# Kernel optimization log

Measured on AMD Instinct MI355X. Metric: run time of the kernel, lower is better.

## Reference

```python
import jax, jax.numpy as jnp
import numpy as np

B = 4; S_L = 512; WIN = 256; SCH = 3; CCH = 128; F = 8; P = 4; RNN = 128; FC = 256
L1 = (WIN - F + 1) // P          # after conv1 + pool1
L2 = (L1 - F + 1) // P           # after conv2 + pool2
D1 = L2 * CCH                    # flattened conv feature dim fed to GRU


def _conv1d(x, w, b):
    # x: (N, W, Cin), w: (F, Cin, Cout), VALID, stride 1 (matches keras Conv1D)
    return jax.lax.conv_general_dilated(x, w, (1,), 'VALID', dimension_numbers=('NWC', 'WIO', 'NWC')) + b


def _maxpool(x, p):
    return jax.lax.reduce_window(x, -jnp.inf, jax.lax.max, (1, p, 1), (1, p, 1), 'VALID')


def _gru(x, h0, mask, W, U, b):
    # keras GRU v2 (reset_after=True). b[0]=input bias, b[1]=recurrent bias.
    # Masked steps carry state through (keras semantics: output==state for GRU).
    u = U.shape[0]
    xg = x @ W + b[0]  # (B, T, 3u) precomputed input projections
    br = b[1]

    def step(h, inp):
        xt, mt = inp  # (B, 3u), (B,)
        rg = h @ U + br
        z = jax.nn.sigmoid(xt[:, :u] + rg[:, :u])
        r = jax.nn.sigmoid(xt[:, u:2 * u] + rg[:, u:2 * u])
        hh = jnp.tanh(xt[:, 2 * u:] + r * rg[:, 2 * u:])
        hn = z * h + (1.0 - z) * hh
        hn = jnp.where(mt[:, None], hn, h)
        return hn, hn

    _, ys = jax.lax.scan(step, h0, (jnp.swapaxes(xg, 0, 1), jnp.swapaxes(mask, 0, 1)))
    return jnp.swapaxes(ys, 0, 1)  # (B, T, u)


def _bidir(x, m, hf, hb, Wf, Uf, bf, Wb, Ub, bb):
    # Bidirectional(merge='concat'); backward layer sees reversed inputs+mask,
    # its output is reversed back to align with time (keras behaviour).
    yf = _gru(x, hf, m, Wf, Uf, bf)
    yb = _gru(x[:, ::-1], hb, m[:, ::-1], Wb, Ub, bb)[:, ::-1]
    return jnp.concatenate([yf, yb], axis=-1)


def _forward(x, state1_f, state1_b, state2_f, state2_b,
             conv1_w, conv1_b, conv2_w, conv2_b,
             g1f_W, g1f_U, g1f_b, g1b_W, g1b_U, g1b_b,
             g2f_W, g2f_U, g2f_b, g2b_W, g2b_U, g2b_b,
             d1_w, d1_b, d2_w, d2_b, d3_w, d3_b, m):
    bsz = x.shape[0]
    h = x.reshape(bsz * S_L, WIN, SCH)
    h = _maxpool(jax.nn.leaky_relu(_conv1d(h, conv1_w, conv1_b), 0.2), P)
    h = _maxpool(jax.nn.leaky_relu(_conv1d(h, conv2_w, conv2_b), 0.2), P)
    h = h.reshape(bsz, S_L, D1)
    h = _bidir(h, m, state1_f, state1_b, g1f_W, g1f_U, g1f_b, g1b_W, g1b_U, g1b_b)
    h = _bidir(h, m, state2_f, state2_b, g2f_W, g2f_U, g2f_b, g2b_W, g2b_U, g2b_b)
    # keras layers.Attention(use_scale=False): dot-product self attention,
    # key mask -> -1e9 on scores, query mask -> zero outputs.
    scores = jnp.einsum('btd,bsd->bts', h, h)
    scores = jnp.where(m[:, None, :], scores, -1e9)
    h = jnp.einsum('bts,bsd->btd', jax.nn.softmax(scores, axis=-1), h)
    h = h * m[:, :, None].astype(h.dtype)
    h = jax.nn.leaky_relu(h @ d1_w + d1_b, 0.2)   # dropout is identity at inference
    h = jax.nn.leaky_relu(h @ d2_w + d2_b, 0.2)
    return (h @ d3_w + d3_b)[..., 0]              # squeeze -> (B, s_l)


def setup_inputs() -> dict:
    key = jax.random.key(0)
    ks = jax.random.split(key, 32)
    g = lambda k, s: jax.random.normal(k, s, jnp.float32) * 0.05
    inp = {}
    inp['x'] = jax.random.normal(ks[0], (B, S_L, WIN, SCH), jnp.float32)
    inp['m'] = jax.random.randint(ks[1], (B, S_L), 0, 2) > 0
    inp['state1_f'] = jax.random.uniform(ks[2], (B, RNN), jnp.float32, -1.0, 1.0)
    inp['state1_b'] = jax.random.uniform(ks[3], (B, RNN), jnp.float32, -1.0, 1.0)
    inp['state2_f'] = jax.random.uniform(ks[4], (B, RNN), jnp.float32, -1.0, 1.0)
    inp['state2_b'] = jax.random.uniform(ks[5], (B, RNN), jnp.float32, -1.0, 1.0)
    inp['conv1_w'] = g(ks[6], (F, SCH, CCH)); inp['conv1_b'] = jnp.zeros((CCH,), jnp.float32)
    inp['conv2_w'] = g(ks[7], (F, CCH, CCH)); inp['conv2_b'] = jnp.zeros((CCH,), jnp.float32)
    i = 8
    for nm, din in (('g1f', D1), ('g1b', D1), ('g2f', 2 * RNN), ('g2b', 2 * RNN)):
        inp[nm + '_W'] = g(ks[i], (din, 3 * RNN))
        inp[nm + '_U'] = g(ks[i + 1], (RNN, 3 * RNN))
        inp[nm + '_b'] = jnp.zeros((2, 3 * RNN), jnp.float32)
        i += 2
    inp['d1_w'] = g(ks[i], (2 * RNN, FC)); inp['d1_b'] = jnp.zeros((FC,), jnp.float32)
    inp['d2_w'] = g(ks[i + 1], (FC, FC)); inp['d2_b'] = jnp.zeros((FC,), jnp.float32)
    inp['d3_w'] = g(ks[i + 2], (FC, 1)); inp['d3_b'] = jnp.zeros((1,), jnp.float32)
    return inp


def reference(x, m, state1_f, state1_b, state2_f, state2_b,
              conv1_w, conv1_b, conv2_w, conv2_b,
              g1f_W, g1f_U, g1f_b, g1b_W, g1b_U, g1b_b,
              g2f_W, g2f_U, g2f_b, g2b_W, g2b_U, g2b_b,
              d1_w, d1_b, d2_w, d2_b, d3_w, d3_b):
    return _forward(x, state1_f, state1_b, state2_f, state2_b,
                    conv1_w, conv1_b, conv2_w, conv2_b,
                    g1f_W, g1f_U, g1f_b, g1b_W, g1b_U, g1b_b,
                    g2f_W, g2f_U, g2f_b, g2b_W, g2b_U, g2b_b,
                    d1_w, d1_b, d2_w, d2_b, d3_w, d3_b, m)
```

## Files before the change

### kernel.cpp

```cpp
#include <hip/hip_runtime.h>

#define LRELU(v) ((v) > 0.f ? (v) : 0.2f * (v))

typedef float f32x4 __attribute__((ext_vector_type(4)));
typedef __bf16 bf16x8 __attribute__((ext_vector_type(8)));
typedef unsigned short ushort8v __attribute__((ext_vector_type(8)));
typedef unsigned int u32x2 __attribute__((ext_vector_type(2)));

__device__ __forceinline__ unsigned short f2bf(float f) {
    unsigned int u = __float_as_uint(f);
    u += 0x7fffu + ((u >> 16) & 1u);
    return (unsigned short)(u >> 16);
}
__device__ __forceinline__ float bf2f(unsigned short h) {
    return __uint_as_float(((unsigned int)h) << 16);
}
__device__ __forceinline__ float sigmoid_fast(float x) {
    float e = __builtin_amdgcn_exp2f(-x * 1.442695041f);
    return __builtin_amdgcn_rcpf(1.f + e);
}
__device__ __forceinline__ float tanh_fast(float x) {
    float e = __builtin_amdgcn_exp2f(x * 2.885390082f);
    return 1.f - 2.f * __builtin_amdgcn_rcpf(e + 1.f);
}
__device__ __forceinline__ float dpp_add_xor1(float v) {
    int r = __builtin_amdgcn_mov_dpp(__float_as_int(v), 0xB1, 0xF, 0xF, true);
    return v + __int_as_float(r);
}
__device__ __forceinline__ float dpp_add_xor2(float v) {
    int r = __builtin_amdgcn_mov_dpp(__float_as_int(v), 0x4E, 0xF, 0xF, true);
    return v + __int_as_float(r);
}

__device__ __forceinline__ void wtpack(const float* __restrict__ W,
                                       unsigned short* __restrict__ h,
                                       unsigned short* __restrict__ l, int K,
                                       int N, long idx) {
    int n = (int)(idx / K), k = (int)(idx % K);
    float v = W[(long)k * N + n];
    unsigned short hi = f2bf(v);
    h[idx] = hi;
    l[idx] = f2bf(v - bf2f(hi));
}
__device__ __forceinline__ void ugpack(const float* __restrict__ U,
                                       float* __restrict__ up, int widx) {
    int t = widx / 96;
    int rem = widx % 96;
    int j = rem >> 2, i = rem & 3;
    int g = j >> 3, q = j & 7;
    int c = t >> 2, kq = t & 3;
    up[widx] = U[(long)(kq * 32 + q * 4 + i) * 384 + g * 128 + c];
}

__global__ __launch_bounds__(256) void prepack_all(
    const float* __restrict__ w2, unsigned short* __restrict__ bth,
    unsigned short* __restrict__ btl, const float* __restrict__ g1fW,
    unsigned short* __restrict__ wt1fh, unsigned short* __restrict__ wt1fl,
    const float* __restrict__ g1bW, unsigned short* __restrict__ wt1bh,
    unsigned short* __restrict__ wt1bl, const float* __restrict__ g2fW,
    unsigned short* __restrict__ wt2fh, unsigned short* __restrict__ wt2fl,
    const float* __restrict__ g2bW, unsigned short* __restrict__ wt2bh,
    unsigned short* __restrict__ wt2bl, const float* __restrict__ g1fU,
    float* __restrict__ up1f, const float* __restrict__ g1bU,
    float* __restrict__ up1b, const float* __restrict__ g2fU,
    float* __restrict__ up2f, const float* __restrict__ g2bU,
    float* __restrict__ up2b, const unsigned int* __restrict__ mraw,
    int* __restrict__ mi) {
    const int bid = blockIdx.x, tid = threadIdx.x;
    if (bid < 512) {
        int idx = bid * 256 + tid;
        int c = idx >> 10, k = idx & 1023;
        float v = w2[k * 128 + c];
        unsigned short hi = f2bf(v);
        bth[(long)c * 1024 + k] = hi;
        btl[(long)c * 1024 + k] = f2bf(v - bf2f(hi));
    } else if (bid < 3008) {
        wtpack(g1fW, wt1fh, wt1fl, 1664, 384, (long)(bid - 512) * 256 + tid);
    } else if (bid < 5504) {
        wtpack(g1bW, wt1bh, wt1bl, 1664, 384, (long)(bid - 3008) * 256 + tid);
    } else if (bid < 5888) {
        wtpack(g2fW, wt2fh, wt2fl, 256, 384, (long)(bid - 5504) * 256 + tid);
    } else if (bid < 6272) {
        wtpack(g2bW, wt2bh, wt2bl, 256, 384, (long)(bid - 5888) * 256 + tid);
    } else if (bid < 6464) {
        ugpack(g1fU, up1f, (bid - 6272) * 256 + tid);
    } else if (bid < 6656) {
        ugpack(g1bU, up1b, (bid - 6464) * 256 + tid);
    } else if (bid < 6848) {
        ugpack(g2fU, up2f, (bid - 6656) * 256 + tid);
    } else if (bid < 7040) {
        ugpack(g2bU, up2b, (bid - 6848) * 256 + tid);
    } else {
        __shared__ int flag;
        if (tid == 0) flag = 0;
        __syncthreads();
        unsigned a = mraw[tid * 2], bb = mraw[tid * 2 + 1];
        if (a > 1u || bb > 1u) flag = 1;
        __syncthreads();
        if (flag) {
            const unsigned char* b8 = (const unsigned char*)mraw;
            for (int i = tid; i < 2048; i += 256) mi[i] = b8[i] ? 1 : 0;
        } else {
            for (int i = tid; i < 2048; i += 256) mi[i] = mraw[i] ? 1 : 0;
        }
    }
}

__global__ __launch_bounds__(256) void conv_kernel(
    const float* __restrict__ x, const float* __restrict__ w1,
    const float* __restrict__ b1, const unsigned short* __restrict__ bth,
    const unsigned short* __restrict__ btl, const float* __restrict__ b2,
    unsigned short* __restrict__ feat_h, unsigned short* __restrict__ feat_l) {
    __shared__ float xs[3][256];
    __shared__ __align__(16) unsigned short p1h[72 * 128];
    __shared__ __align__(16) unsigned short p1l[72 * 128];
    long s = blockIdx.x;
    int tid = threadIdx.x;
    const float* xp = x + s * 768;
    for (int i = tid; i < 768; i += 256) xs[i % 3][i / 3] = xp[i];
    for (int i = tid; i < 10 * 128; i += 256) {
        p1h[62 * 128 + i] = 0;
        p1l[62 * 128 + i] = 0;
    }
    __syncthreads();

    {
        int ch = tid & 127;
        int half = tid >> 7;
        float w1r[24];
#pragma unroll
        for (int fc = 0; fc < 24; fc++) w1r[fc] = w1[fc * 128 + ch];
        float bias1 = b1[ch];
        for (int po = half; po < 62; po += 2) {
            int p0 = po * 4;
            float a0 = bias1, a1 = bias1, a2 = bias1, a3 = bias1;
#pragma unroll
            for (int c = 0; c < 3; c++) {
                float xv[11];
#pragma unroll
                for (int q = 0; q < 11; q++) xv[q] = xs[c][p0 + q];
#pragma unroll
                for (int f = 0; f < 8; f++) {
                    float w = w1r[f * 3 + c];
                    a0 = fmaf(xv[f + 0], w, a0);
                    a1 = fmaf(xv[f + 1], w, a1);
                    a2 = fmaf(xv[f + 2], w, a2);
                    a3 = fmaf(xv[f + 3], w, a3);
                }
            }
            float m01 = fmaxf(LRELU(a0), LRELU(a1));
            float m23 = fmaxf(LRELU(a2), LRELU(a3));
            float v = fmaxf(m01, m23);
            unsigned short hi = f2bf(v);
            unsigned short lo = f2bf(v - bf2f(hi));
            int cs = ch ^ ((po & 7) << 3);
            p1h[po * 128 + cs] = hi;
            p1l[po * 128 + cs] = lo;
        }
    }
    __syncthreads();

    const int l = tid & 63, w = tid >> 6;
    const int r = l & 15, g = l >> 4;
    f32x4 acc[4][2];
    const f32x4 zz = {0.f, 0.f, 0.f, 0.f};
#pragma unroll
    for (int m = 0; m < 4; m++) {
        acc[m][0] = zz;
        acc[m][1] = zz;
    }
#pragma unroll 2
    for (int ks = 0; ks < 32; ks++) {
        const int f = ks >> 2;
        const int cin0 = ((ks & 3) << 5) + (g << 3);
        bf16x8 bh[2], bl[2];
#pragma unroll
        for (int n = 0; n < 2; n++) {
            const int c = ((w << 1) + n) * 16 + r;
            const long bo = (long)c * 1024 + (ks << 5) + (g << 3);
            bh[n] = __builtin_bit_cast(bf16x8, *(const ushort8v*)(bth + bo));
            bl[n] = __builtin_bit_cast(bf16x8, *(const ushort8v*)(btl + bo));
        }
        bf16x8 ah[4], al[4];
#pragma unroll
        for (int m = 0; m < 4; m++) {
            const int row = m * 16 + r + f;
            const int col = cin0 ^ ((row & 7) << 3);
            const int off = row * 128 + col;
            ah[m] = __builtin_bit_cast(bf16x8, *(const ushort8v*)(p1h + off));
            al[m] = __builtin_bit_cast(bf16x8, *(const ushort8v*)(p1l + off));
        }
#pragma unroll
        for (int m = 0; m < 4; m++) {
#pragma unroll
            for (int n = 0; n < 2; n++) {
                acc[m][n] = __builtin_amdgcn_mfma_f32_16x16x32_bf16(ah[m], bh[n], acc[m][n], 0, 0, 0);
                acc[m][n] = __builtin_amdgcn_mfma_f32_16x16x32_bf16(ah[m], bl[n], acc[m][n], 0, 0, 0);
                acc[m][n] = __builtin_amdgcn_mfma_f32_16x16x32_bf16(al[m], bh[n], acc[m][n], 0, 0, 0);
            }
        }
    }
#pragma unroll
    for (int m = 0; m < 4; m++) {
        const int j = m * 4 + g;
        if (j < 13) {
#pragma unroll
            for (int n = 0; n < 2; n++) {
                const int ch = ((w << 1) + n) * 16 + r;
                const float bias = b2[ch];
                float v0 = LRELU(acc[m][n].x + bias);
                float v1 = LRELU(acc[m][n].y + bias);
                float v2 = LRELU(acc[m][n].z + bias);
                float v3 = LRELU(acc[m][n].w + bias);
                float v = fmaxf(fmaxf(v0, v1), fmaxf(v2, v3));
                unsigned short hi = f2bf(v);
                feat_h[s * 1664 + j * 128 + ch] = hi;
                feat_l[s * 1664 + j * 128 + ch] = f2bf(v - bf2f(hi));
            }
        }
    }
}

__global__ __launch_bounds__(256) void gemm_proj(
    const unsigned short* __restrict__ Agh, const unsigned short* __restrict__ Agl,
    const unsigned short* __restrict__ B0h, const unsigned short* __restrict__ B0l,
    const unsigned short* __restrict__ B1h, const unsigned short* __restrict__ B1l,
    const float* __restrict__ bias0, const float* __restrict__ bias1,
    float* __restrict__ C0, float* __restrict__ C1, int M, int N, int K) {
    const int z = blockIdx.z;
    const unsigned short* __restrict__ Bth = z ? B1h : B0h;
    const unsigned short* __restrict__ Btl = z ? B1l : B0l;
    const float* __restrict__ bias = z ? bias1 : bias0;
    float* __restrict__ C = z ? C1 : C0;
    __shared__ __align__(16) unsigned short Ahs[2][64 * 32];
    __shared__ __align__(16) unsigned short Als[2][64 * 32];
    const int tid = threadIdx.x;
    const int w = tid >> 6, l = tid & 63, r = l & 15, g = l >> 4;
    const int m0 = blockIdx.y * 64, n0 = blockIdx.x * 64;
    const int col = n0 + w * 16 + r;
    const int srow = tid >> 2, sgq = tid & 3;
    f32x4 acc[4];
    const f32x4 zzv = {0.f, 0.f, 0.f, 0.f};
#pragma unroll
    for (int m = 0; m < 4; m++) acc[m] = zzv;

    const long abase = (long)(m0 + srow) * K + ((sgq ^ (srow & 3)) << 3);
    auto stage = [&](int k0, int buf) {
        __builtin_amdgcn_global_load_lds(
            (const __attribute__((address_space(1))) void*)(Agh + abase + k0),
            (__attribute__((address_space(3))) void*)&Ahs[buf][tid * 8], 16, 0, 0);
        __builtin_amdgcn_global_load_lds(
            (const __attribute__((address_space(1))) void*)(Agl + abase + k0),
            (__attribute__((address_space(3))) void*)&Als[buf][tid * 8], 16, 0, 0);
    };
    stage(0, 0);
    const long bbase = (long)col * K + g * 8;
    ushort8v bhc = *(const ushort8v*)(Bth + bbase);
    ushort8v blc = *(const ushort8v*)(Btl + bbase);

    for (int k0 = 0; k0 < K; k0 += 32) {
        const int buf = (k0 >> 5) & 1;
        asm volatile("s_waitcnt vmcnt(0)" ::: "memory");
        __builtin_amdgcn_s_barrier();
        ushort8v nbh, nbl;
        if (k0 + 32 < K) {
            stage(k0 + 32, buf ^ 1);
            nbh = *(const ushort8v*)(Bth + bbase + k0 + 32);
            nbl = *(const ushort8v*)(Btl + bbase + k0 + 32);
        }
        bf16x8 bh = __builtin_bit_cast(bf16x8, bhc);
        bf16x8 bl = __builtin_bit_cast(bf16x8, blc);
#pragma unroll
        for (int m = 0; m < 4; m++) {
            const int arow = m * 16 + r;
            const int aoff = arow * 32 + ((g ^ (arow & 3)) << 3);
            bf16x8 ah = __builtin_bit_cast(bf16x8, *(const ushort8v*)(&Ahs[buf][aoff]));
            bf16x8 al = __builtin_bit_cast(bf16x8, *(const ushort8v*)(&Als[buf][aoff]));
            acc[m] = __builtin_amdgcn_mfma_f32_16x16x32_bf16(ah, bh, acc[m], 0, 0, 0);
            acc[m] = __builtin_amdgcn_mfma_f32_16x16x32_bf16(ah, bl, acc[m], 0, 0, 0);
            acc[m] = __builtin_amdgcn_mfma_f32_16x16x32_bf16(al, bh, acc[m], 0, 0, 0);
        }
        bhc = nbh;
        blc = nbl;
    }
    const float bv = bias[col];
#pragma unroll
    for (int m = 0; m < 4; m++) {
#pragma unroll
        for (int q = 0; q < 4; q++) {
            const int row = m0 + m * 16 + g * 4 + q;
            C[(long)row * N + col] = acc[m][q] + bv;
        }
    }
}

__global__ __launch_bounds__(256) void gemm_scores(
    const unsigned short* __restrict__ Hh, const unsigned short* __restrict__ Hl,
    const int* __restrict__ mask, float* __restrict__ S) {
    const int bz = blockIdx.z;
    const unsigned short* __restrict__ Agh = Hh + (long)bz * 512 * 256;
    const unsigned short* __restrict__ Agl = Hl + (long)bz * 512 * 256;
    float* __restrict__ C = S + (long)bz * 512 * 512;
    const int K = 256, N = 512;
    __shared__ __align__(16) unsigned short Ahs[2][64 * 32];
    __shared__ __align__(16) unsigned short Als[2][64 * 32];
    const int tid = threadIdx.x;
    const int w = tid >> 6, l = tid & 63, r = l & 15, g = l >> 4;
    const int m0 = blockIdx.y * 64, n0 = blockIdx.x * 64;
    const int col = n0 + w * 16 + r;
    const int srow = tid >> 2, sgq = tid & 3;
    f32x4 acc[4];
    const f32x4 zzv = {0.f, 0.f, 0.f, 0.f};
#pragma unroll
    for (int m = 0; m < 4; m++) acc[m] = zzv;

    const long abase = (long)(m0 + srow) * K + ((sgq ^ (srow & 3)) << 3);
    auto stage = [&](int k0, int buf) {
        __builtin_amdgcn_global_load_lds(
            (const __attribute__((address_space(1))) void*)(Agh + abase + k0),
            (__attribute__((address_space(3))) void*)&Ahs[buf][tid * 8], 16, 0, 0);
        __builtin_amdgcn_global_load_lds(
            (const __attribute__((address_space(1))) void*)(Agl + abase + k0),
            (__attribute__((address_space(3))) void*)&Als[buf][tid * 8], 16, 0, 0);
    };
    stage(0, 0);
    const long bbase = (long)col * K + g * 8;
    ushort8v bhc = *(const ushort8v*)(Agh + bbase);
    ushort8v blc = *(const ushort8v*)(Agl + bbase);

    for (int k0 = 0; k0 < K; k0 += 32) {
        const int buf = (k0 >> 5) & 1;
        asm volatile("s_waitcnt vmcnt(0)" ::: "memory");
        __builtin_amdgcn_s_barrier();
        ushort8v nbh, nbl;
        if (k0 + 32 < K) {
            stage(k0 + 32, buf ^ 1);
            nbh = *(const ushort8v*)(Agh + bbase + k0 + 32);
            nbl = *(const ushort8v*)(Agl + bbase + k0 + 32);
        }
        bf16x8 bh = __builtin_bit_cast(bf16x8, bhc);
        bf16x8 bl = __builtin_bit_cast(bf16x8, blc);
#pragma unroll
        for (int m = 0; m < 4; m++) {
            const int arow = m * 16 + r;
            const int aoff = arow * 32 + ((g ^ (arow & 3)) << 3);
            bf16x8 ah = __builtin_bit_cast(bf16x8, *(const ushort8v*)(&Ahs[buf][aoff]));
            bf16x8 al = __builtin_bit_cast(bf16x8, *(const ushort8v*)(&Als[buf][aoff]));
            acc[m] = __builtin_amdgcn_mfma_f32_16x16x32_bf16(ah, bh, acc[m], 0, 0, 0);
            acc[m] = __builtin_amdgcn_mfma_f32_16x16x32_bf16(ah, bl, acc[m], 0, 0, 0);
            acc[m] = __builtin_amdgcn_mfma_f32_16x16x32_bf16(al, bh, acc[m], 0, 0, 0);
        }
        bhc = nbh;
        blc = nbl;
    }
    const int mk = mask[bz * 512 + col];
#pragma unroll
    for (int m = 0; m < 4; m++) {
#pragma unroll
        for (int q = 0; q < 4; q++) {
            const int row = m0 + m * 16 + g * 4 + q;
            float v = acc[m][q];
            C[(long)row * N + col] = mk ? v : -1e9f;
        }
    }
}

template <int ACT>
__global__ __launch_bounds__(256) void gemm_nn(
    const float* __restrict__ A, long sA, const float* __restrict__ B, long sB,
    const float* __restrict__ bias, const int* __restrict__ qmask,
    float* __restrict__ C, long sC, int M, int N, int K) {
    int bz = blockIdx.z;
    A += (long)bz * sA;
    B += (long)bz * sB;
    C += (long)bz * sC;
    __shared__ __align__(16) float As[16][68];
    __shared__ __align__(16) float Bs[16][68];
    int tid = threadIdx.x;
    int tm = tid >> 4, tn = tid & 15;
    int m0 = blockIdx.y * 64, n0 = blockIdx.x * 64;
    int la_m = tid & 63, la_k = (tid >> 6) * 4;
    int lb_k = tid >> 4, lb_n = (tid & 15) * 4;
    float acc[4][4] = {};
    for (int k0 = 0; k0 < K; k0 += 16) {
        float4 av = *(const float4*)&A[(long)(m0 + la_m) * K + k0 + la_k];
        float4 bv = *(const float4*)&B[(long)(k0 + lb_k) * N + n0 + lb_n];
        As[la_k + 0][la_m] = av.x;
        As[la_k + 1][la_m] = av.y;
        As[la_k + 2][la_m] = av.z;
        As[la_k + 3][la_m] = av.w;
        *(float4*)&Bs[lb_k][lb_n] = bv;
        __syncthreads();
#pragma unroll
        for (int k = 0; k < 16; k++) {
            float4 a4 = *(const float4*)&As[k][tm * 4];
            float4 b4 = *(const float4*)&Bs[k][tn * 4];
            float aa[4] = {a4.x, a4.y, a4.z, a4.w};
            float bb[4] = {b4.x, b4.y, b4.z, b4.w};
#pragma unroll
            for (int i = 0; i < 4; i++)
#pragma unroll
                for (int j = 0; j < 4; j++) acc[i][j] = fmaf(aa[i], bb[j], acc[i][j]);
        }
        __syncthreads();
    }
#pragma unroll
    for (int i = 0; i < 4; i++) {
        int row = m0 + tm * 4 + i;
        float msc = qmask ? (float)qmask[(long)bz * M + row] : 1.f;
#pragma unroll
        for (int j = 0; j < 4; j++) {
            int col = n0 + tn * 4 + j;
            float v = acc[i][j] + (bias ? bias[col] : 0.f);
            if (ACT == 1) v = LRELU(v);
            C[(long)row * N + col] = v * msc;
        }
    }
}

__global__ __launch_bounds__(256) void softmax_kernel(float* __restrict__ S) {
    long row = blockIdx.x;
    float* p = S + row * 512;
    int tid = threadIdx.x;
    __shared__ float red[8];
    float v0 = p[tid], v1 = p[tid + 256];
    float mx = fmaxf(v0, v1);
#pragma unroll
    for (int off = 32; off; off >>= 1) mx = fmaxf(mx, __shfl_down(mx, off));
    if ((tid & 63) == 0) red[tid >> 6] = mx;
    __syncthreads();
    mx = fmaxf(fmaxf(red[0], red[1]), fmaxf(red[2], red[3]));
    float e0 = expf(v0 - mx), e1 = expf(v1 - mx);
    float sm = e0 + e1;
#pragma unroll
    for (int off = 32; off; off >>= 1) sm += __shfl_down(sm, off);
    if ((tid & 63) == 0) red[4 + (tid >> 6)] = sm;
    __syncthreads();
    float inv = 1.f / (red[4] + red[5] + red[6] + red[7]);
    p[tid] = e0 * inv;
    p[tid + 256] = e1 * inv;
}

#define D4(a0, a1, hv, uv)           \
    a0 = fmaf(hv.x, uv.x, a0);       \
    a1 = fmaf(hv.y, uv.y, a1);       \
    a0 = fmaf(hv.z, uv.z, a0);       \
    a1 = fmaf(hv.w, uv.w, a1);

#define LOADU(dst, offs)                                             \
    asm volatile("global_load_dwordx4 %0, %1, off offset:" #offs     \
                 : "=&v"(dst)                                        \
                 : "v"(ub)                                           \
                 : "memory")

template <int WF32>
__global__ __launch_bounds__(512, 2) void gru_kernel(
    const float* __restrict__ xgf, const float* __restrict__ xgb,
    const float* __restrict__ Upf, const float* __restrict__ Upb,
    const float* __restrict__ brf, const float* __restrict__ brb,
    const float* __restrict__ h0f, const float* __restrict__ h0b,
    const int* __restrict__ mask, float* __restrict__ out,
    unsigned short* __restrict__ outh, unsigned short* __restrict__ outl) {
    int b = blockIdx.x & 3;
    int dir = blockIdx.x >> 2;
    const float* __restrict__ xg = dir ? xgb : xgf;
    const float* __restrict__ Up = dir ? Upb : Upf;
    const float* __restrict__ br = dir ? brb : brf;
    const float* __restrict__ h0 = dir ? h0b : h0f;
    const int tid = threadIdx.x;
    const int c = tid >> 2;
    const int kq = tid & 3;

    __shared__ __align__(16) float xs[2][16 * 384];
    __shared__ __align__(16) float hsh[2][144];
    __shared__ __align__(16) unsigned int histp[16][128];
    __shared__ __align__(16) float histf[16][128];
    __shared__ unsigned long long mwords[8];

    const float* ub = Up + (long)tid * 96;
    f32x4 uz0, uz1, uz2, uz3, uz4, uz5, uz6, uz7;
    f32x4 ur0, ur1, ur2, ur3, ur4, ur5, ur6, ur7;
    f32x4 uh0, uh1, uh2, uh3, uh4, uh5, uh6, uh7;
    LOADU(uz0, 0);   LOADU(uz1, 16);  LOADU(uz2, 32);  LOADU(uz3, 48);
    LOADU(uz4, 64);  LOADU(uz5, 80);  LOADU(uz6, 96);  LOADU(uz7, 112);
    LOADU(ur0, 128); LOADU(ur1, 144); LOADU(ur2, 160); LOADU(ur3, 176);
    LOADU(ur4, 192); LOADU(ur5, 208); LOADU(ur6, 224); LOADU(ur7, 240);
    LOADU(uh0, 256); LOADU(uh1, 272); LOADU(uh2, 288); LOADU(uh3, 304);
    LOADU(uh4, 320); LOADU(uh5, 336); LOADU(uh6, 352); LOADU(uh7, 368);
    asm volatile("s_waitcnt vmcnt(0)" ::: "memory");
    __builtin_amdgcn_sched_barrier(0);

    auto stage = [&](int cc, int bufi) {
#pragma unroll
        for (int i = 0; i < 3; i++) {
            int g = i * 512 + tid;
            int j = g / 96;
            int col = (g - j * 96) * 4;
            int ts = cc * 16 + j;
            int t = dir ? (511 - ts) : ts;
            const float* src = xg + ((long)(b * 512 + t)) * 384 + col;
            __builtin_amdgcn_global_load_lds(
                (const __attribute__((address_space(1))) void*)src,
                (__attribute__((address_space(3))) void*)&xs[bufi][g * 4], 16, 0, 0);
        }
    };
    stage(0, 0);

    float br3[3];
#pragma unroll
    for (int g = 0; g < 3; g++) br3[g] = br[g * 128 + c];

    float hreg = h0[b * 128 + c];
    if (kq == 0) hsh[0][c + (c >> 5) * 4] = hreg;
    if (tid < 64) {
#pragma unroll
        for (int w = 0; w < 8; w++) {
            int idx = w * 64 + tid;
            int t = dir ? (511 - idx) : idx;
            unsigned long long bm = __ballot(mask[b * 512 + t] != 0);
            if (tid == 0) mwords[w] = bm;
        }
    }
    asm volatile("s_waitcnt lgkmcnt(0)" ::: "memory");
    __builtin_amdgcn_s_barrier();

    int cur = 0;
    for (int cc = 0; cc < 32; cc++) {
        asm volatile("s_waitcnt vmcnt(0)" ::: "memory");
        if (cc < 31) stage(cc + 1, (cc + 1) & 1);
        __builtin_amdgcn_s_barrier();
        const float* xb = xs[cc & 1];
        unsigned mwbits = (unsigned)((mwords[cc >> 2] >> ((cc & 3) * 16)) & 0xffffull);
#pragma unroll 1
        for (int jj = 0; jj < 16; jj++) {
            if ((mwbits >> jj) & 1) {
                const float* hp = &hsh[cur][kq * 36];
                float4 h0v = *(const float4*)(hp + 0);
                float4 h1v = *(const float4*)(hp + 4);
                float4 h2v = *(const float4*)(hp + 8);
                float4 h3v = *(const float4*)(hp + 12);
                float4 h4v = *(const float4*)(hp + 16);
                float4 h5v = *(const float4*)(hp + 20);
                float4 h6v = *(const float4*)(hp + 24);
                float4 h7v = *(const float4*)(hp + 28);
                float az0 = 0.f, az1 = 0.f, ar0 = 0.f, ar1 = 0.f, ah0 = 0.f, ah1 = 0.f;
                D4(az0, az1, h0v, uz0) D4(az0, az1, h1v, uz1)
                D4(az0, az1, h2v, uz2) D4(az0, az1, h3v, uz3)
                D4(az0, az1, h4v, uz4) D4(az0, az1, h5v, uz5)
                D4(az0, az1, h6v, uz6) D4(az0, az1, h7v, uz7)
                D4(ar0, ar1, h0v, ur0) D4(ar0, ar1, h1v, ur1)
                D4(ar0, ar1, h2v, ur2) D4(ar0, ar1, h3v, ur3)
                D4(ar0, ar1, h4v, ur4) D4(ar0, ar1, h5v, ur5)
                D4(ar0, ar1, h6v, ur6) D4(ar0, ar1, h7v, ur7)
                D4(ah0, ah1, h0v, uh0) D4(ah0, ah1, h1v, uh1)
                D4(ah0, ah1, h2v, uh2) D4(ah0, ah1, h3v, uh3)
                D4(ah0, ah1, h4v, uh4) D4(ah0, ah1, h5v, uh5)
                D4(ah0, ah1, h6v, uh6) D4(ah0, ah1, h7v, uh7)
                float rgz = dpp_add_xor2(dpp_add_xor1(az0 + az1));
                float rgr = dpp_add_xor2(dpp_add_xor1(ar0 + ar1));
                float rgh = dpp_add_xor2(dpp_add_xor1(ah0 + ah1));
                if (kq == 0) {
                    float xz = xb[jj * 384 + c];
                    float xr = xb[jj * 384 + 128 + c];
                    float xh = xb[jj * 384 + 256 + c];
                    float z = sigmoid_fast(xz + rgz + br3[0]);
                    float r_ = sigmoid_fast(xr + rgr + br3[1]);
                    float hc = tanh_fast(fmaf(r_, rgh + br3[2], xh));
                    float hn = fmaf(z, hreg - hc, hc);
                    hreg = hn;
                    hsh[cur ^ 1][c + (c >> 5) * 4] = hn;
                    if (WF32) histf[jj][c] = hn;
                    unsigned short hh = f2bf(hn);
                    histp[jj][c] = (unsigned)hh |
                                   ((unsigned)f2bf(hn - bf2f(hh)) << 16);
                }
                asm volatile("s_waitcnt lgkmcnt(0)" ::: "memory");
                __builtin_amdgcn_s_barrier();
                cur ^= 1;
            } else {
                if (kq == 0) {
                    if (WF32) histf[jj][c] = hreg;
                    unsigned short hh = f2bf(hreg);
                    histp[jj][c] = (unsigned)hh |
                                   ((unsigned)f2bf(hreg - bf2f(hh)) << 16);
                }
            }
        }
        asm volatile("s_waitcnt lgkmcnt(0)" ::: "memory");
        __builtin_amdgcn_s_barrier();
        {
            int fj = tid >> 5, fc = (tid & 31) << 2;
            int ts2 = cc * 16 + fj;
            int tf = dir ? (511 - ts2) : ts2;
            long ob = ((long)(b * 512 + tf)) * 256 + dir * 128 + fc;
            uint4 hp4 = *(const uint4*)&histp[fj][fc];
            u32x2 ph, pl;
            ph.x = (hp4.x & 0xffffu) | (hp4.y << 16);
            ph.y = (hp4.z & 0xffffu) | (hp4.w << 16);
            pl.x = (hp4.x >> 16) | (hp4.y & 0xffff0000u);
            pl.y = (hp4.z >> 16) | (hp4.w & 0xffff0000u);
            *(u32x2*)(outh + ob) = ph;
            *(u32x2*)(outl + ob) = pl;
            if (WF32) *(float4*)(out + ob) = *(const float4*)&histf[fj][fc];
        }
    }
}

__global__ __launch_bounds__(256) void final_kernel(
    const float* __restrict__ fc2, const float* __restrict__ w,
    const float* __restrict__ b, float* __restrict__ out) {
    int row = blockIdx.x * 4 + (threadIdx.x >> 6);
    int lane = threadIdx.x & 63;
    const float* a = fc2 + (long)row * 256;
    float acc = 0.f;
#pragma unroll
    for (int i = 0; i < 4; i++) acc = fmaf(a[lane + i * 64], w[lane + i * 64], acc);
#pragma unroll
    for (int off = 32; off; off >>= 1) acc += __shfl_down(acc, off);
    if (lane == 0) out[row] = acc + b[0];
}

extern "C" void kernel_launch(void* const* d_in, const int* in_sizes, int n_in,
                              void* d_out, int out_size, void* d_ws,
                              size_t ws_size, hipStream_t stream) {
    const float* x = (const float*)d_in[0];
    const unsigned int* mraw = (const unsigned int*)d_in[1];
    const float* s1f = (const float*)d_in[2];
    const float* s1b = (const float*)d_in[3];
    const float* s2f = (const float*)d_in[4];
    const float* s2b = (const float*)d_in[5];
    const float* c1w = (const float*)d_in[6];
    const float* c1b = (const float*)d_in[7];
    const float* c2w = (const float*)d_in[8];
    const float* c2b = (const float*)d_in[9];
    const float* g1fW = (const float*)d_in[10];
    const float* g1fU = (const float*)d_in[11];
    const float* g1fb = (const float*)d_in[12];
    const float* g1bW = (const float*)d_in[13];
    const float* g1bU = (const float*)d_in[14];
    const float* g1bb = (const float*)d_in[15];
    const float* g2fW = (const float*)d_in[16];
    const float* g2fU = (const float*)d_in[17];
    const float* g2fb = (const float*)d_in[18];
    const float* g2bW = (const float*)d_in[19];
    const float* g2bU = (const float*)d_in[20];
    const float* g2bb = (const float*)d_in[21];
    const float* d1w = (const float*)d_in[22];
    const float* d1b = (const float*)d_in[23];
    const float* d2w = (const float*)d_in[24];
    const float* d2b = (const float*)d_in[25];
    const float* d3w = (const float*)d_in[26];
    const float* d3b = (const float*)d_in[27];
    float* out = (float*)d_out;

    float* ws = (float*)d_ws;
    size_t off = 0;
    auto take = [&](size_t n) {
        float* p = ws + off;
        off += (n + 63) & ~(size_t)63;
        return p;
    };
    int* mask_i = (int*)take(2048);
    unsigned short* feat_h = (unsigned short*)take(2048UL * 1664 / 2);
    unsigned short* feat_l = (unsigned short*)take(2048UL * 1664 / 2);
    float* xg1f = take(2048UL * 384);
    float* xg1b = take(2048UL * 384);
    unsigned short* gru1h = (unsigned short*)take(2048UL * 128);
    unsigned short* gru1l = (unsigned short*)take(2048UL * 128);
    float* xg2f = take(2048UL * 384);
    float* xg2b = take(2048UL * 384);
    float* gru2 = take(2048UL * 256);
    unsigned short* gru2h = (unsigned short*)take(2048UL * 128);
    unsigned short* gru2l = (unsigned short*)take(2048UL * 128);
    float* sc = take(4UL * 512 * 512);
    float* attn = take(2048UL * 256);
    float* fc1 = take(2048UL * 256);
    float* fc2 = take(2048UL * 256);
    unsigned short* bth = (unsigned short*)take(65536);
    unsigned short* btl = (unsigned short*)take(65536);
    unsigned short* wt1fh = (unsigned short*)take(319488);
    unsigned short* wt1fl = (unsigned short*)take(319488);
    unsigned short* wt1bh = (unsigned short*)take(319488);
    unsigned short* wt1bl = (unsigned short*)take(319488);
    unsigned short* wt2fh = (unsigned short*)take(49152);
    unsigned short* wt2fl = (unsigned short*)take(49152);
    unsigned short* wt2bh = (unsigned short*)take(49152);
    unsigned short* wt2bl = (unsigned short*)take(49152);
    float* up1f = take(49152);
    float* up1b = take(49152);
    float* up2f = take(49152);
    float* up2b = take(49152);

    prepack_all<<<7041, 256, 0, stream>>>(
        c2w, bth, btl, g1fW, wt1fh, wt1fl, g1bW, wt1bh, wt1bl, g2fW, wt2fh,
        wt2fl, g2bW, wt2bh, wt2bl, g1fU, up1f, g1bU, up1b, g2fU, up2f, g2bU,
        up2b, mraw, mask_i);
    conv_kernel<<<2048, 256, 0, stream>>>(x, c1w, c1b, bth, btl, c2b, feat_h, feat_l);

    gemm_proj<<<dim3(6, 32, 2), 256, 0, stream>>>(
        feat_h, feat_l, wt1fh, wt1fl, wt1bh, wt1bl, g1fb, g1bb, xg1f, xg1b,
        2048, 384, 1664);
    gru_kernel<0><<<8, 512, 0, stream>>>(xg1f, xg1b, up1f, up1b, g1fb + 384,
                                         g1bb + 384, s1f, s1b, mask_i, nullptr,
                                         gru1h, gru1l);

    gemm_proj<<<dim3(6, 32, 2), 256, 0, stream>>>(
        gru1h, gru1l, wt2fh, wt2fl, wt2bh, wt2bl, g2fb, g2bb, xg2f, xg2b,
        2048, 384, 256);
    gru_kernel<1><<<8, 512, 0, stream>>>(xg2f, xg2b, up2f, up2b, g2fb + 384,
                                         g2bb + 384, s2f, s2b, mask_i, gru2,
                                         gru2h, gru2l);

    gemm_scores<<<dim3(8, 8, 4), 256, 0, stream>>>(gru2h, gru2l, mask_i, sc);
    softmax_kernel<<<2048, 256, 0, stream>>>(sc);
    gemm_nn<0><<<dim3(4, 8, 4), 256, 0, stream>>>(sc, 512L * 512, gru2, 512L * 256,
                                                  nullptr, mask_i, attn, 512L * 256,
                                                  512, 256, 512);

    gemm_nn<1><<<dim3(4, 32, 1), 256, 0, stream>>>(attn, 0, d1w, 0, d1b, nullptr,
                                                   fc1, 0, 2048, 256, 256);
    gemm_nn<1><<<dim3(4, 32, 1), 256, 0, stream>>>(fc1, 0, d2w, 0, d2b, nullptr,
                                                   fc2, 0, 2048, 256, 256);
    final_kernel<<<512, 256, 0, stream>>>(fc2, d3w, d3b, out);
}
```

Before: 678.1 us.

## Split GRU recurrent matvec across eight lanes per hidden unit with 1024-thread blocks

The GRU recurrent kernel now runs 1024 threads per block, with eight threads cooperating on each hidden unit instead of four. Each thread holds 48 recurrent weights in registers instead of 96. The U prepack layout, the hidden-state padding and the final writeback are changed to match. The aim is a shorter serial per-step dot-product chain, at the cost of an extra cross-lane shuffle reduction per gate and more waves synchronizing at each barrier.

```diff
diff --git a/kernel.cpp b/kernel.cpp
--- a/kernel.cpp
+++ b/kernel.cpp
@@ -5,7 +5,6 @@
 typedef float f32x4 __attribute__((ext_vector_type(4)));
 typedef __bf16 bf16x8 __attribute__((ext_vector_type(8)));
 typedef unsigned short ushort8v __attribute__((ext_vector_type(8)));
-typedef unsigned int u32x2 __attribute__((ext_vector_type(2)));
 
 __device__ __forceinline__ unsigned short f2bf(float f) {
     unsigned int u = __float_as_uint(f);
@@ -44,12 +43,12 @@
 }
 __device__ __forceinline__ void ugpack(const float* __restrict__ U,
                                        float* __restrict__ up, int widx) {
-    int t = widx / 96;
-    int rem = widx % 96;
-    int j = rem >> 2, i = rem & 3;
-    int g = j >> 3, q = j & 7;
-    int c = t >> 2, kq = t & 3;
-    up[widx] = U[(long)(kq * 32 + q * 4 + i) * 384 + g * 128 + c];
+    int t = widx / 48;
+    int rem = widx % 48;
+    int g = rem >> 4, rem2 = rem & 15;
+    int q = rem2 >> 2, i = rem2 & 3;
+    int c = t >> 3, kq = t & 7;
+    up[widx] = U[(long)(kq * 16 + q * 4 + i) * 384 + g * 128 + c];
 }
 
 __global__ __launch_bounds__(256) void prepack_all(
@@ -447,14 +446,8 @@
     a0 = fmaf(hv.z, uv.z, a0);       \
     a1 = fmaf(hv.w, uv.w, a1);
 
-#define LOADU(dst, offs)                                             \
-    asm volatile("global_load_dwordx4 %0, %1, off offset:" #offs     \
-                 : "=&v"(dst)                                        \
-                 : "v"(ub)                                           \
-                 : "memory")
-
 template <int WF32>
-__global__ __launch_bounds__(512, 2) void gru_kernel(
+__global__ __launch_bounds__(1024, 4) void gru_kernel(
     const float* __restrict__ xgf, const float* __restrict__ xgb,
     const float* __restrict__ Upf, const float* __restrict__ Upb,
     const float* __restrict__ brf, const float* __restrict__ brb,
@@ -468,8 +461,8 @@
     const float* __restrict__ br = dir ? brb : brf;
     const float* __restrict__ h0 = dir ? h0b : h0f;
     const int tid = threadIdx.x;
-    const int c = tid >> 2;
-    const int kq = tid & 3;
+    const int c = tid >> 3;
+    const int kq = tid & 7;
 
     __shared__ __align__(16) float xs[2][16 * 384];
     __shared__ __align__(16) float hsh[2][144];
@@ -477,41 +470,37 @@
     __shared__ __align__(16) float histf[16][128];
     __shared__ unsigned long long mwords[8];
 
-    const float* ub = Up + (long)tid * 96;
-    f32x4 uz0, uz1, uz2, uz3, uz4, uz5, uz6, uz7;
-    f32x4 ur0, ur1, ur2, ur3, ur4, ur5, ur6, ur7;
-    f32x4 uh0, uh1, uh2, uh3, uh4, uh5, uh6, uh7;
-    LOADU(uz0, 0);   LOADU(uz1, 16);  LOADU(uz2, 32);  LOADU(uz3, 48);
-    LOADU(uz4, 64);  LOADU(uz5, 80);  LOADU(uz6, 96);  LOADU(uz7, 112);
-    LOADU(ur0, 128); LOADU(ur1, 144); LOADU(ur2, 160); LOADU(ur3, 176);
-    LOADU(ur4, 192); LOADU(ur5, 208); LOADU(ur6, 224); LOADU(ur7, 240);
-    LOADU(uh0, 256); LOADU(uh1, 272); LOADU(uh2, 288); LOADU(uh3, 304);
-    LOADU(uh4, 320); LOADU(uh5, 336); LOADU(uh6, 352); LOADU(uh7, 368);
-    asm volatile("s_waitcnt vmcnt(0)" ::: "memory");
-    __builtin_amdgcn_sched_barrier(0);
-
     auto stage = [&](int cc, int bufi) {
 #pragma unroll
-        for (int i = 0; i < 3; i++) {
-            int g = i * 512 + tid;
-            int j = g / 96;
-            int col = (g - j * 96) * 4;
-            int ts = cc * 16 + j;
-            int t = dir ? (511 - ts) : ts;
-            const float* src = xg + ((long)(b * 512 + t)) * 384 + col;
-            __builtin_amdgcn_global_load_lds(
-                (const __attribute__((address_space(1))) void*)src,
-                (__attribute__((address_space(3))) void*)&xs[bufi][g * 4], 16, 0, 0);
+        for (int i = 0; i < 2; i++) {
+            int g = i * 1024 + tid;
+            if (g < 1536) {
+                int j = g / 96;
+                int col = (g - j * 96) * 4;
+                int ts = cc * 16 + j;
+                int t = dir ? (511 - ts) : ts;
+                const float* src = xg + ((long)(b * 512 + t)) * 384 + col;
+                __builtin_amdgcn_global_load_lds(
+                    (const __attribute__((address_space(1))) void*)src,
+                    (__attribute__((address_space(3))) void*)&xs[bufi][g * 4], 16, 0, 0);
+            }
         }
     };
     stage(0, 0);
 
+    f32x4 u4[12];
+    {
+        const f32x4* up = (const f32x4*)(Up + (long)tid * 48);
+#pragma unroll
+        for (int q = 0; q < 12; q++) u4[q] = up[q];
+    }
+
     float br3[3];
 #pragma unroll
     for (int g = 0; g < 3; g++) br3[g] = br[g * 128 + c];
 
     float hreg = h0[b * 128 + c];
-    if (kq == 0) hsh[0][c + (c >> 5) * 4] = hreg;
+    if (kq == 0) hsh[0][c + (c >> 4) * 2] = hreg;
     if (tid < 64) {
 #pragma unroll
         for (int w = 0; w < 8; w++) {
@@ -534,31 +523,24 @@
 #pragma unroll 1
         for (int jj = 0; jj < 16; jj++) {
             if ((mwbits >> jj) & 1) {
-                const float* hp = &hsh[cur][kq * 36];
+                const float* hp = &hsh[cur][kq * 18];
                 float4 h0v = *(const float4*)(hp + 0);
                 float4 h1v = *(const float4*)(hp + 4);
                 float4 h2v = *(const float4*)(hp + 8);
                 float4 h3v = *(const float4*)(hp + 12);
-                float4 h4v = *(const float4*)(hp + 16);
-                float4 h5v = *(const float4*)(hp + 20);
-                float4 h6v = *(const float4*)(hp + 24);
-                float4 h7v = *(const float4*)(hp + 28);
                 float az0 = 0.f, az1 = 0.f, ar0 = 0.f, ar1 = 0.f, ah0 = 0.f, ah1 = 0.f;
-                D4(az0, az1, h0v, uz0) D4(az0, az1, h1v, uz1)
-                D4(az0, az1, h2v, uz2) D4(az0, az1, h3v, uz3)
-                D4(az0, az1, h4v, uz4) D4(az0, az1, h5v, uz5)
-                D4(az0, az1, h6v, uz6) D4(az0, az1, h7v, uz7)
-                D4(ar0, ar1, h0v, ur0) D4(ar0, ar1, h1v, ur1)
-                D4(ar0, ar1, h2v, ur2) D4(ar0, ar1, h3v, ur3)
-                D4(ar0, ar1, h4v, ur4) D4(ar0, ar1, h5v, ur5)
-                D4(ar0, ar1, h6v, ur6) D4(ar0, ar1, h7v, ur7)
-                D4(ah0, ah1, h0v, uh0) D4(ah0, ah1, h1v, uh1)
-                D4(ah0, ah1, h2v, uh2) D4(ah0, ah1, h3v, uh3)
-                D4(ah0, ah1, h4v, uh4) D4(ah0, ah1, h5v, uh5)
-                D4(ah0, ah1, h6v, uh6) D4(ah0, ah1, h7v, uh7)
+                D4(az0, az1, h0v, u4[0]) D4(az0, az1, h1v, u4[1])
+                D4(az0, az1, h2v, u4[2]) D4(az0, az1, h3v, u4[3])
+                D4(ar0, ar1, h0v, u4[4]) D4(ar0, ar1, h1v, u4[5])
+                D4(ar0, ar1, h2v, u4[6]) D4(ar0, ar1, h3v, u4[7])
+                D4(ah0, ah1, h0v, u4[8]) D4(ah0, ah1, h1v, u4[9])
+                D4(ah0, ah1, h2v, u4[10]) D4(ah0, ah1, h3v, u4[11])
                 float rgz = dpp_add_xor2(dpp_add_xor1(az0 + az1));
                 float rgr = dpp_add_xor2(dpp_add_xor1(ar0 + ar1));
                 float rgh = dpp_add_xor2(dpp_add_xor1(ah0 + ah1));
+                rgz += __shfl_xor(rgz, 4);
+                rgr += __shfl_xor(rgr, 4);
+                rgh += __shfl_xor(rgh, 4);
                 if (kq == 0) {
                     float xz = xb[jj * 384 + c];
                     float xr = xb[jj * 384 + 128 + c];
@@ -568,7 +550,7 @@
                     float hc = tanh_fast(fmaf(r_, rgh + br3[2], xh));
                     float hn = fmaf(z, hreg - hc, hc);
                     hreg = hn;
-                    hsh[cur ^ 1][c + (c >> 5) * 4] = hn;
+                    hsh[cur ^ 1][c + (c >> 4) * 2] = hn;
                     if (WF32) histf[jj][c] = hn;
                     unsigned short hh = f2bf(hn);
                     histp[jj][c] = (unsigned)hh |
@@ -589,19 +571,14 @@
         asm volatile("s_waitcnt lgkmcnt(0)" ::: "memory");
         __builtin_amdgcn_s_barrier();
         {
-            int fj = tid >> 5, fc = (tid & 31) << 2;
+            int fj = tid >> 6, fc = (tid & 63) << 1;
             int ts2 = cc * 16 + fj;
             int tf = dir ? (511 - ts2) : ts2;
             long ob = ((long)(b * 512 + tf)) * 256 + dir * 128 + fc;
-            uint4 hp4 = *(const uint4*)&histp[fj][fc];
-            u32x2 ph, pl;
-            ph.x = (hp4.x & 0xffffu) | (hp4.y << 16);
-            ph.y = (hp4.z & 0xffffu) | (hp4.w << 16);
-            pl.x = (hp4.x >> 16) | (hp4.y & 0xffff0000u);
-            pl.y = (hp4.z >> 16) | (hp4.w & 0xffff0000u);
-            *(u32x2*)(outh + ob) = ph;
-            *(u32x2*)(outl + ob) = pl;
-            if (WF32) *(float4*)(out + ob) = *(const float4*)&histf[fj][fc];
+            unsigned p0 = histp[fj][fc], p1 = histp[fj][fc + 1];
+            *(unsigned*)(outh + ob) = (p0 & 0xffffu) | (p1 << 16);
+            *(unsigned*)(outl + ob) = (p0 >> 16) | (p1 & 0xffff0000u);
+            if (WF32) *(float2*)(out + ob) = *(const float2*)&histf[fj][fc];
         }
     }
 }
@@ -700,16 +677,16 @@
     gemm_proj<<<dim3(6, 32, 2), 256, 0, stream>>>(
         feat_h, feat_l, wt1fh, wt1fl, wt1bh, wt1bl, g1fb, g1bb, xg1f, xg1b,
         2048, 384, 1664);
-    gru_kernel<0><<<8, 512, 0, stream>>>(xg1f, xg1b, up1f, up1b, g1fb + 384,
-                                         g1bb + 384, s1f, s1b, mask_i, nullptr,
-                                         gru1h, gru1l);
+    gru_kernel<0><<<8, 1024, 0, stream>>>(xg1f, xg1b, up1f, up1b, g1fb + 384,
+                                          g1bb + 384, s1f, s1b, mask_i, nullptr,
+                                          gru1h, gru1l);
 
     gemm_proj<<<dim3(6, 32, 2), 256, 0, stream>>>(
         gru1h, gru1l, wt2fh, wt2fl, wt2bh, wt2bl, g2fb, g2bb, xg2f, xg2b,
         2048, 384, 256);
-    gru_kernel<1><<<8, 512, 0, stream>>>(xg2f, xg2b, up2f, up2b, g2fb + 384,
-                                         g2bb + 384, s2f, s2b, mask_i, gru2,
-                                         gru2h, gru2l);
+    gru_kernel<1><<<8, 1024, 0, stream>>>(xg2f, xg2b, up2f, up2b, g2fb + 384,
+                                          g2bb + 384, s2f, s2b, mask_i, gru2,
+                                          gru2h, gru2l);
 
     gemm_scores<<<dim3(8, 8, 4), 256, 0, stream>>>(gru2h, gru2l, mask_i, sc);
     softmax_kernel<<<2048, 256, 0, stream>>>(sc);
```

Result: slower. 1.565 ms (+130.8%).
